# Optimization experiments

Hardware: AMD Instinct MI355X
Metric: run time of the kernel (lower is better)

## Reference

```python
import jax, jax.numpy as jnp
import numpy as np

N_EMB = 1024
N_HEADS = 16
HS = N_EMB // N_HEADS  # 64
BASE = 10000.0


def _rope_cache(T):
    # theta uses dim = n_emb (as in the source), sliced to hs//2 frequencies
    i = jnp.arange(HS // 2, dtype=jnp.float32)
    theta = BASE ** (-2.0 * i / N_EMB)            # [hs/2]
    pos = jnp.arange(T, dtype=jnp.float32)        # [T]
    ang = pos[:, None] * theta[None, :]           # [T, hs/2]
    return jnp.cos(ang), jnp.sin(ang)


def _apply_rope(x, cos, sin):
    # x: [B, T, nh, hs]; rotate consecutive pairs along hs
    b, t, nh, hs = x.shape
    xr = x.reshape(b, t, nh, hs // 2, 2)
    c = cos[None, :, None, :]
    s = sin[None, :, None, :]
    r0 = xr[..., 0] * c - xr[..., 1] * s
    r1 = xr[..., 1] * c + xr[..., 0] * s
    return jnp.stack([r0, r1], axis=-1).reshape(b, t, nh, hs)


def setup_inputs() -> dict:
    key = jax.random.key(0)
    k1, k2, k3, k4 = jax.random.split(key, 4)
    B, T = 2, 2048
    w_std = 0.02
    x = jax.random.normal(k1, (B, T, N_EMB), jnp.float32)
    Wq = jax.random.normal(k2, (N_EMB, N_EMB), jnp.float32) * w_std
    Wk = jax.random.normal(k3, (N_EMB, N_EMB), jnp.float32) * w_std
    Wv = jax.random.normal(k4, (N_EMB, N_EMB), jnp.float32) * w_std
    return {"x": x, "Wq": Wq, "Wk": Wk, "Wv": Wv}


def reference(x, Wq, Wk, Wv):
    B, T, C = x.shape
    # nn.Linear(bias=False): y = x @ W.T
    q = (x @ Wq.T).reshape(B, T, N_HEADS, HS)
    k = (x @ Wk.T).reshape(B, T, N_HEADS, HS)
    v = (x @ Wv.T).reshape(B, T, N_HEADS, HS)
    cos, sin = _rope_cache(T)
    q = _apply_rope(q, cos, sin)
    k = _apply_rope(k, cos, sin)
    # scale uses C (n_emb), as in the source (not head_size)
    wei = jnp.einsum('bqhd,bkhd->bhqk', q, k) * (C ** -0.5)  # [B, nh, T, T]
    mask = jnp.tril(jnp.ones((T, T), dtype=bool))
    wei = jnp.where(mask[None, None], wei, -jnp.inf)
    wei = jax.nn.softmax(wei, axis=-1)
    # dropout is identity in eval mode
    out = jnp.einsum('bhqk,bkhd->bqhd', wei, v).reshape(B, T, C)
    return out
```

## Files before the change

### kernel.cpp

```cpp
#include <hip/hip_runtime.h>
#include <stdint.h>

typedef unsigned short u16;
typedef __bf16 bf16x8 __attribute__((ext_vector_type(8)));
typedef unsigned short u16x8 __attribute__((ext_vector_type(8)));
typedef float f32x4 __attribute__((ext_vector_type(4)));
typedef uint32_t u32v4 __attribute__((ext_vector_type(4)));

#define LOG2E 1.4426950408889634f

typedef const __attribute__((address_space(1))) uint32_t as1_u32;
typedef __attribute__((address_space(3))) uint32_t as3_u32;

__device__ __forceinline__ u16 f2bf(float f) {
  union { float f; uint32_t i; } v; v.f = f;
  uint32_t r = (v.i + 0x7fffu + ((v.i >> 16) & 1u)) >> 16;
  return (u16)r;
}
__device__ __forceinline__ float bf2f(u16 u) {
  union { uint32_t i; float f; } v; v.i = ((uint32_t)u) << 16; return v.f;
}

__device__ __forceinline__ void gld_lds16(const void* g, void* l) {
  as1_u32* gp = (as1_u32*)((uintptr_t)g);
  as3_u32* lp = (as3_u32*)(uint32_t)(uintptr_t)(l);
  __builtin_amdgcn_global_load_lds(gp, lp, 16, 0, 0);
}

__device__ __forceinline__ float fast_exp2(float x) {
  float r;
  asm("v_exp_f32 %0, %1" : "=v"(r) : "v"(x));
  return r;
}

__global__ __launch_bounds__(256) void f32_to_bf16(
    const float* __restrict__ x, const float* __restrict__ wq,
    const float* __restrict__ wk, const float* __restrict__ wv,
    u16* __restrict__ xc, u16* __restrict__ wqc,
    u16* __restrict__ wkc, u16* __restrict__ wvc) {
  const int z = blockIdx.y;
  const float* src = z == 0 ? x : (z == 1 ? wq : (z == 2 ? wk : wv));
  u16* dst = z == 0 ? xc : (z == 1 ? wqc : (z == 2 ? wkc : wvc));
  const int n = z == 0 ? (1 << 22) : (1 << 20);

  const int idx = (blockIdx.x * 256 + (int)threadIdx.x) * 8;
  if (idx >= n) return;
  const f32x4 a = *(const f32x4*)&src[idx];
  const f32x4 b = *(const f32x4*)&src[idx + 4];
  u16x8 o;
#pragma unroll
  for (int j = 0; j < 4; j++) { o[j] = f2bf(a[j]); o[j + 4] = f2bf(b[j]); }
  *(u16x8*)&dst[idx] = o;
}

__global__ __launch_bounds__(256) void qkv_gemm(
    const u16* __restrict__ xc, const u16* __restrict__ wqc,
    const u16* __restrict__ wkc, const u16* __restrict__ wvc,
    u16* __restrict__ qo, u16* __restrict__ ko, u16* __restrict__ vt) {
  __shared__ __align__(16) u16 As[128 * 64];
  __shared__ __align__(16) u16 Bs[128 * 64];

  const int tid = threadIdx.x;
  const int lane = tid & 63;
  const int w = tid >> 6;
  const int wm = w >> 1, wn = w & 1;
  const int quad = lane >> 4, m16 = lane & 15;
  const int which = blockIdx.z;

  const u16* __restrict__ Ap;
  const u16* __restrict__ Bp;
  int m0, n0;
  if (which == 2) {
    Ap = wvc; Bp = xc;
    m0 = blockIdx.x * 128;
    n0 = blockIdx.y * 128;
  } else {
    Ap = xc; Bp = which == 0 ? wqc : wkc;
    m0 = blockIdx.y * 128;
    n0 = blockIdx.x * 128;
  }

  const f32x4 z4 = {0.f, 0.f, 0.f, 0.f};
  f32x4 acc[4][4];
#pragma unroll
  for (int i = 0; i < 4; i++)
#pragma unroll
    for (int j = 0; j < 4; j++) acc[i][j] = z4;

  const int lrow = lane >> 3;
  const int scol = ((lane & 7) ^ (lrow & 7)) * 8;
  const int srowA = m0 + w * 32 + lrow;
  const int srowB = n0 + w * 32 + lrow;
  const int rsw = m16 & 7;

  for (int k0 = 0; k0 < 1024; k0 += 64) {
    __syncthreads();
#pragma unroll
    for (int j = 0; j < 4; j++) {
      gld_lds16(&Ap[(size_t)(srowA + j * 8) * 1024 + k0 + scol],
                &As[(w * 32 + j * 8) * 64]);
      gld_lds16(&Bp[(size_t)(srowB + j * 8) * 1024 + k0 + scol],
                &Bs[(w * 32 + j * 8) * 64]);
    }
    __syncthreads();

#pragma unroll
    for (int kk = 0; kk < 2; kk++) {
      bf16x8 af[4], bfr[4];
#pragma unroll
      for (int t = 0; t < 4; t++) {
        af[t] = *(const bf16x8*)
            &As[(wm * 64 + t * 16 + m16) * 64 + (((kk * 4 + quad) ^ rsw) * 8)];
        bfr[t] = *(const bf16x8*)
            &Bs[(wn * 64 + t * 16 + m16) * 64 + (((kk * 4 + quad) ^ rsw) * 8)];
      }
#pragma unroll
      for (int mt = 0; mt < 4; mt++)
#pragma unroll
        for (int nt = 0; nt < 4; nt++)
          acc[mt][nt] = __builtin_amdgcn_mfma_f32_16x16x32_bf16(
              af[mt], bfr[nt], acc[mt][nt], 0, 0, 0);
    }
  }

  if (which < 2) {
    u16* __restrict__ out = which == 0 ? qo : ko;
    float th[4];
#pragma unroll
    for (int nt = 0; nt < 4; nt++) {
      const int i = ((nt * 16 + m16) & 63) >> 1;
      th[nt] = fast_exp2(-(float)i * 0.02595256324130752f)
               * 0.15915494309189535f;
    }
    const float sgn = (m16 & 1) ? 1.f : -1.f;
#pragma unroll
    for (int mt = 0; mt < 4; mt++) {
      const int row = m0 + wm * 64 + mt * 16 + quad * 4;
#pragma unroll
      for (int nt = 0; nt < 4; nt++) {
        const int n = n0 + wn * 64 + nt * 16 + m16;
        f32x4 a = acc[mt][nt];
#pragma unroll
        for (int r = 0; r < 4; r++) {
          const int t = (row + r) & 2047;
          const float rev = (float)t * th[nt];
          float fr, sv, cv;
          asm("v_fract_f32 %0, %1" : "=v"(fr) : "v"(rev));
          asm("v_sin_f32 %0, %1" : "=v"(sv) : "v"(fr));
          asm("v_cos_f32 %0, %1" : "=v"(cv) : "v"(fr));
          const float own = a[r];
          const float other = __shfl_xor(own, 1);
          out[(size_t)(row + r) * 1024 + n] = f2bf(own * cv + other * (sgn * sv));
        }
      }
    }
  } else {
    const int m16p = (m16 & 3) | ((m16 & 4) << 1) | ((m16 & 8) >> 1);
#pragma unroll
    for (int mt = 0; mt < 4; mt++) {
      const int row = m0 + wm * 64 + mt * 16 + quad * 4;
#pragma unroll
      for (int nt = 0; nt < 4; nt++) {
        const int n = n0 + wn * 64 + nt * 16 + m16p;
        f32x4 a = acc[mt][nt];
#pragma unroll
        for (int r = 0; r < 4; r++)
          vt[(size_t)(row + r) * 4096 + n] = f2bf(a[r]);
      }
    }
  }
}

__global__ __launch_bounds__(256, 2) void flash_attn(
    const u16* __restrict__ qg, const u16* __restrict__ kg,
    const u16* __restrict__ vt, float* __restrict__ out) {
  __shared__ __align__(16) u16 Ks[128 * 72];
  __shared__ __align__(16) u16 Vs[64 * 136];

  const int tid = threadIdx.x, lane = tid & 63, w = tid >> 6;
  const int quad = lane >> 4, m16 = lane & 15;

  const int id   = (int)blockIdx.x;
  const int X    = id & 7;
  const int rem  = id >> 3;
  const int s    = rem & 1;
  const int vloc = (rem >> 1) & 3;
  const int kk_  = rem >> 3;
  const int Q    = s ? 15 - kk_ : kk_;
  const int v    = X * 4 + vloc;
  const int h    = v & 15;
  const int b    = v >> 4;

  const size_t base  = (size_t)b * 2048 * 1024 + (size_t)h * 64;
  const size_t vbase = (size_t)(h * 64) * 4096 + (size_t)b * 2048;
  const float SC = 0.03125f * LOG2E;
  const f32x4 z4 = {0.f, 0.f, 0.f, 0.f};
  const int srow = tid >> 2, sc = (tid & 3) * 16;

  union { u16x8 u; bf16x8 f; } ones;
#pragma unroll
  for (int k = 0; k < 8; k++) ones.u[k] = 0x3F80;

  const int q0 = Q * 128;
  const int nr = Q + 1;

  const u16* qsA = &qg[base + (size_t)(q0 + w * 32 + m16) * 1024 + quad * 8];
  const bf16x8 qfA0 = *(const bf16x8*)qsA;
  const bf16x8 qfA1 = *(const bf16x8*)(qsA + 32);
  const u16* qsB = qsA + (size_t)16 * 1024;
  const bf16x8 qfB0 = *(const bf16x8*)qsB;
  const bf16x8 qfB1 = *(const bf16x8*)(qsB + 32);

  u16x8 kr0, kr1, kr2, kr3, vr0, vr1, vr2, vr3;
  {
    const u16* ks = &kg[base + (size_t)srow * 1024 + sc];
    kr0 = *(const u16x8*)ks; kr1 = *(const u16x8*)(ks + 8);
    const u16* ks2 = ks + (size_t)64 * 1024;
    kr2 = *(const u16x8*)ks2; kr3 = *(const u16x8*)(ks2 + 8);
    const u16* vs = &vt[vbase + (size_t)srow * 4096 + sc];
    vr0 = *(const u16x8*)vs; vr1 = *(const u16x8*)(vs + 8);
    vr2 = *(const u16x8*)(vs + 64); vr3 = *(const u16x8*)(vs + 72);
  }

  f32x4 lA = z4, lB = z4;
  f32x4 OA[4], OB[4];
#pragma unroll
  for (int d = 0; d < 4; d++) { OA[d] = z4; OB[d] = z4; }

  const int qrowA = q0 + w * 32 + quad * 4;
  const int qcolA = q0 + w * 32 + m16;

  for (int rr = 0; rr < nr; ++rr) {
    const int k0 = rr * 128;
    if (rr) __syncthreads();
    *(u16x8*)&Ks[srow * 72 + sc] = kr0;
    *(u16x8*)&Ks[srow * 72 + sc + 8] = kr1;
    *(u16x8*)&Ks[(64 + srow) * 72 + sc] = kr2;
    *(u16x8*)&Ks[(64 + srow) * 72 + sc + 8] = kr3;
    *(u16x8*)&Vs[srow * 136 + sc] = vr0;
    *(u16x8*)&Vs[srow * 136 + sc + 8] = vr1;
    *(u16x8*)&Vs[srow * 136 + 64 + sc] = vr2;
    *(u16x8*)&Vs[srow * 136 + 64 + sc + 8] = vr3;
    __syncthreads();
    if (rr + 1 < nr) {
      const u16* ks = &kg[base + (size_t)(k0 + 128 + srow) * 1024 + sc];
      kr0 = *(const u16x8*)ks; kr1 = *(const u16x8*)(ks + 8);
      const u16* ks2 = ks + (size_t)64 * 1024;
      kr2 = *(const u16x8*)ks2; kr3 = *(const u16x8*)(ks2 + 8);
      const u16* vs = &vt[vbase + (size_t)srow * 4096 + k0 + 128 + sc];
      vr0 = *(const u16x8*)vs; vr1 = *(const u16x8*)(vs + 8);
      vr2 = *(const u16x8*)(vs + 64); vr3 = *(const u16x8*)(vs + 72);
    }

    f32x4 SA[8], SB[8];
#pragma unroll
    for (int nt = 0; nt < 8; nt++) {
      const bf16x8 kf0 = *(const bf16x8*)&Ks[(nt * 16 + m16) * 72 + quad * 8];
      const bf16x8 kf1 =
          *(const bf16x8*)&Ks[(nt * 16 + m16) * 72 + 32 + quad * 8];
      SA[nt] = __builtin_amdgcn_mfma_f32_16x16x32_bf16(kf0, qfA0, z4, 0, 0, 0);
      SA[nt] = __builtin_amdgcn_mfma_f32_16x16x32_bf16(kf1, qfA1, SA[nt], 0, 0, 0);
      SB[nt] = __builtin_amdgcn_mfma_f32_16x16x32_bf16(kf0, qfB0, z4, 0, 0, 0);
      SB[nt] = __builtin_amdgcn_mfma_f32_16x16x32_bf16(kf1, qfB1, SB[nt], 0, 0, 0);
    }

    const bool lastr = (rr == nr - 1);

    union { u32v4 u; bf16x8 f; } PA[4], PB[4];
    {
      uint32_t W[16];
#pragma unroll
      for (int nt = 0; nt < 8; nt++) {
        float p[4];
#pragma unroll
        for (int r = 0; r < 4; r++) {
          float e = fast_exp2(SA[nt][r] * SC);
          const int key = k0 + nt * 16 + quad * 4 + r;
          if (lastr && key > qcolA) e = 0.f;
          p[r] = e;
        }
        uint32_t w0, w1;
        asm("v_cvt_pk_bf16_f32 %0, %1, %2" : "=v"(w0) : "v"(p[0]), "v"(p[1]));
        asm("v_cvt_pk_bf16_f32 %0, %1, %2" : "=v"(w1) : "v"(p[2]), "v"(p[3]));
        W[2 * nt] = w0; W[2 * nt + 1] = w1;
      }
#pragma unroll
      for (int ks = 0; ks < 4; ks++) {
        uint32_t a0 = W[4 * ks], b0 = W[4 * ks + 2];
        uint32_t a1 = W[4 * ks + 1], b1 = W[4 * ks + 3];
        asm("v_permlane32_swap_b32 %0, %1" : "+v"(a0), "+v"(b0));
        asm("v_permlane32_swap_b32 %0, %1" : "+v"(a1), "+v"(b1));
        PA[ks].u = (u32v4){a0, a1, b0, b1};
      }
    }
    {
      const int qcolB = qcolA + 16;
      uint32_t W[16];
#pragma unroll
      for (int nt = 0; nt < 8; nt++) {
        float p[4];
#pragma unroll
        for (int r = 0; r < 4; r++) {
          float e = fast_exp2(SB[nt][r] * SC);
          const int key = k0 + nt * 16 + quad * 4 + r;
          if (lastr && key > qcolB) e = 0.f;
          p[r] = e;
        }
        uint32_t w0, w1;
        asm("v_cvt_pk_bf16_f32 %0, %1, %2" : "=v"(w0) : "v"(p[0]), "v"(p[1]));
        asm("v_cvt_pk_bf16_f32 %0, %1, %2" : "=v"(w1) : "v"(p[2]), "v"(p[3]));
        W[2 * nt] = w0; W[2 * nt + 1] = w1;
      }
#pragma unroll
      for (int ks = 0; ks < 4; ks++) {
        uint32_t a0 = W[4 * ks], b0 = W[4 * ks + 2];
        uint32_t a1 = W[4 * ks + 1], b1 = W[4 * ks + 3];
        asm("v_permlane32_swap_b32 %0, %1" : "+v"(a0), "+v"(b0));
        asm("v_permlane32_swap_b32 %0, %1" : "+v"(a1), "+v"(b1));
        PB[ks].u = (u32v4){a0, a1, b0, b1};
      }
    }

#pragma unroll
    for (int ks = 0; ks < 4; ks++) {
      lA = __builtin_amdgcn_mfma_f32_16x16x32_bf16(PA[ks].f, ones.f, lA, 0, 0, 0);
      lB = __builtin_amdgcn_mfma_f32_16x16x32_bf16(PB[ks].f, ones.f, lB, 0, 0, 0);
    }

#pragma unroll
    for (int dt = 0; dt < 4; dt++) {
#pragma unroll
      for (int ks = 0; ks < 4; ks++) {
        const bf16x8 vf =
            *(const bf16x8*)&Vs[(dt * 16 + m16) * 136 + ks * 32 + quad * 8];
        OA[dt] = __builtin_amdgcn_mfma_f32_16x16x32_bf16(PA[ks].f, vf, OA[dt],
                                                         0, 0, 0);
        OB[dt] = __builtin_amdgcn_mfma_f32_16x16x32_bf16(PB[ks].f, vf, OB[dt],
                                                         0, 0, 0);
      }
    }
  }

  float invA[4], invB[4];
#pragma unroll
  for (int r = 0; r < 4; r++) { invA[r] = 1.0f / lA[r]; invB[r] = 1.0f / lB[r]; }

#pragma unroll
  for (int dt = 0; dt < 4; dt++)
#pragma unroll
    for (int r = 0; r < 4; r++) {
      out[base + (size_t)(qrowA + r) * 1024 + dt * 16 + m16] =
          OA[dt][r] * invA[r];
      out[base + (size_t)(qrowA + 16 + r) * 1024 + dt * 16 + m16] =
          OB[dt][r] * invB[r];
    }
}

extern "C" void kernel_launch(void* const* d_in, const int* in_sizes, int n_in,
                              void* d_out, int out_size, void* d_ws, size_t ws_size,
                              hipStream_t stream) {
  const float* x  = (const float*)d_in[0];
  const float* Wq = (const float*)d_in[1];
  const float* Wk = (const float*)d_in[2];
  const float* Wv = (const float*)d_in[3];
  u16* qb  = (u16*)d_ws;
  u16* kb  = qb  + (size_t)4096 * 1024;
  u16* vtw = kb  + (size_t)4096 * 1024;
  u16* xc  = vtw + (size_t)4096 * 1024;
  u16* wqc = xc  + (size_t)4096 * 1024;
  u16* wkc = wqc + (size_t)1024 * 1024;
  u16* wvc = wkc + (size_t)1024 * 1024;

  f32_to_bf16<<<dim3(2048, 4), 256, 0, stream>>>(x, Wq, Wk, Wv,
                                                 xc, wqc, wkc, wvc);
  qkv_gemm<<<dim3(8, 32, 3), 256, 0, stream>>>(xc, wqc, wkc, wvc,
                                               qb, kb, vtw);
  flash_attn<<<dim3(512, 1, 1), 256, 0, stream>>>(qb, kb, vtw, (float*)d_out);
}
```

Baseline: 162.0 us.

## Split RoPE into separate kernel, remap GEMM grid per XCD, double-buffer attention LDS

Three changes. The QKV GEMM now uses a flat 1D grid whose block index is remapped so that consecutive blocks on the same XCD share row panels, aiming at better L2 reuse. RoPE moves out of the GEMM epilogue into a separate in-place elementwise kernel, which drops the per-element sin/cos and shuffle from the GEMM but costs an extra launch and an extra read/write pass over Q and K. Flash attention double-buffers its K/V shared-memory tiles so each iteration needs one barrier instead of two, at the cost of twice the LDS per block, which may affect occupancy.

```diff
diff --git a/kernel.cpp b/kernel.cpp
--- a/kernel.cpp
+++ b/kernel.cpp
@@ -65,19 +65,26 @@
   const int w = tid >> 6;
   const int wm = w >> 1, wn = w & 1;
   const int quad = lane >> 4, m16 = lane & 15;
-  const int which = blockIdx.z;
+
+  const int id    = (int)blockIdx.x;
+  const int xcd   = id & 7;
+  const int local = id >> 3;
+  const int by    = xcd * 4 + (local & 3);
+  const int rest  = local >> 2;
+  const int which = rest % 3;
+  const int bx    = rest / 3;
 
   const u16* __restrict__ Ap;
   const u16* __restrict__ Bp;
   int m0, n0;
   if (which == 2) {
     Ap = wvc; Bp = xc;
-    m0 = blockIdx.x * 128;
-    n0 = blockIdx.y * 128;
+    m0 = bx * 128;
+    n0 = by * 128;
   } else {
     Ap = xc; Bp = which == 0 ? wqc : wkc;
-    m0 = blockIdx.y * 128;
-    n0 = blockIdx.x * 128;
+    m0 = by * 128;
+    n0 = bx * 128;
   }
 
   const f32x4 z4 = {0.f, 0.f, 0.f, 0.f};
@@ -125,14 +132,6 @@
 
   if (which < 2) {
     u16* __restrict__ out = which == 0 ? qo : ko;
-    float th[4];
-#pragma unroll
-    for (int nt = 0; nt < 4; nt++) {
-      const int i = ((nt * 16 + m16) & 63) >> 1;
-      th[nt] = fast_exp2(-(float)i * 0.02595256324130752f)
-               * 0.15915494309189535f;
-    }
-    const float sgn = (m16 & 1) ? 1.f : -1.f;
 #pragma unroll
     for (int mt = 0; mt < 4; mt++) {
       const int row = m0 + wm * 64 + mt * 16 + quad * 4;
@@ -141,17 +140,8 @@
         const int n = n0 + wn * 64 + nt * 16 + m16;
         f32x4 a = acc[mt][nt];
 #pragma unroll
-        for (int r = 0; r < 4; r++) {
-          const int t = (row + r) & 2047;
-          const float rev = (float)t * th[nt];
-          float fr, sv, cv;
-          asm("v_fract_f32 %0, %1" : "=v"(fr) : "v"(rev));
-          asm("v_sin_f32 %0, %1" : "=v"(sv) : "v"(fr));
-          asm("v_cos_f32 %0, %1" : "=v"(cv) : "v"(fr));
-          const float own = a[r];
-          const float other = __shfl_xor(own, 1);
-          out[(size_t)(row + r) * 1024 + n] = f2bf(own * cv + other * (sgn * sv));
-        }
+        for (int r = 0; r < 4; r++)
+          out[(size_t)(row + r) * 1024 + n] = f2bf(a[r]);
       }
     }
   } else {
@@ -171,11 +161,39 @@
   }
 }
 
+__global__ __launch_bounds__(256) void rope_inplace(u16* __restrict__ qb,
+                                                    u16* __restrict__ kb) {
+  u16* buf = blockIdx.y == 0 ? qb : kb;
+  const int p = blockIdx.x * 256 + (int)threadIdx.x;
+  const int e0 = p * 8;
+  const int row = e0 >> 10;
+  const int col0 = e0 & 1023;
+  const int t = row & 2047;
+  const float tf = (float)t;
+
+  u16x8 d = *(const u16x8*)&buf[(size_t)row * 1024 + col0];
+  u16x8 o;
+#pragma unroll
+  for (int j = 0; j < 4; j++) {
+    const int i = ((col0 & 63) >> 1) + j;
+    const float th = fast_exp2(-(float)i * 0.02595256324130752f);
+    const float rev = tf * th * 0.15915494309189535f;
+    float fr, s, c;
+    asm("v_fract_f32 %0, %1" : "=v"(fr) : "v"(rev));
+    asm("v_sin_f32 %0, %1" : "=v"(s) : "v"(fr));
+    asm("v_cos_f32 %0, %1" : "=v"(c) : "v"(fr));
+    const float a0 = bf2f(d[2 * j]), a1 = bf2f(d[2 * j + 1]);
+    o[2 * j]     = f2bf(a0 * c - a1 * s);
+    o[2 * j + 1] = f2bf(a1 * c + a0 * s);
+  }
+  *(u16x8*)&buf[(size_t)row * 1024 + col0] = o;
+}
+
 __global__ __launch_bounds__(256, 2) void flash_attn(
     const u16* __restrict__ qg, const u16* __restrict__ kg,
     const u16* __restrict__ vt, float* __restrict__ out) {
-  __shared__ __align__(16) u16 Ks[128 * 72];
-  __shared__ __align__(16) u16 Vs[64 * 136];
+  __shared__ __align__(16) u16 Ks[2][128 * 72];
+  __shared__ __align__(16) u16 Vs[2][64 * 136];
 
   const int tid = threadIdx.x, lane = tid & 63, w = tid >> 6;
   const int quad = lane >> 4, m16 = lane & 15;
@@ -230,18 +248,19 @@
   const int qrowA = q0 + w * 32 + quad * 4;
   const int qcolA = q0 + w * 32 + m16;
 
+  int p = 0;
   for (int rr = 0; rr < nr; ++rr) {
     const int k0 = rr * 128;
-    if (rr) __syncthreads();
-    *(u16x8*)&Ks[srow * 72 + sc] = kr0;
-    *(u16x8*)&Ks[srow * 72 + sc + 8] = kr1;
-    *(u16x8*)&Ks[(64 + srow) * 72 + sc] = kr2;
-    *(u16x8*)&Ks[(64 + srow) * 72 + sc + 8] = kr3;
-    *(u16x8*)&Vs[srow * 136 + sc] = vr0;
-    *(u16x8*)&Vs[srow * 136 + sc + 8] = vr1;
-    *(u16x8*)&Vs[srow * 136 + 64 + sc] = vr2;
-    *(u16x8*)&Vs[srow * 136 + 64 + sc + 8] = vr3;
-    __syncthreads();
+    u16* ksp = &Ks[p][0];
+    u16* vsp = &Vs[p][0];
+    *(u16x8*)&ksp[srow * 72 + sc] = kr0;
+    *(u16x8*)&ksp[srow * 72 + sc + 8] = kr1;
+    *(u16x8*)&ksp[(64 + srow) * 72 + sc] = kr2;
+    *(u16x8*)&ksp[(64 + srow) * 72 + sc + 8] = kr3;
+    *(u16x8*)&vsp[srow * 136 + sc] = vr0;
+    *(u16x8*)&vsp[srow * 136 + sc + 8] = vr1;
+    *(u16x8*)&vsp[srow * 136 + 64 + sc] = vr2;
+    *(u16x8*)&vsp[srow * 136 + 64 + sc + 8] = vr3;
     if (rr + 1 < nr) {
       const u16* ks = &kg[base + (size_t)(k0 + 128 + srow) * 1024 + sc];
       kr0 = *(const u16x8*)ks; kr1 = *(const u16x8*)(ks + 8);
@@ -251,13 +270,14 @@
       vr0 = *(const u16x8*)vs; vr1 = *(const u16x8*)(vs + 8);
       vr2 = *(const u16x8*)(vs + 64); vr3 = *(const u16x8*)(vs + 72);
     }
+    __syncthreads();
 
     f32x4 SA[8], SB[8];
 #pragma unroll
     for (int nt = 0; nt < 8; nt++) {
-      const bf16x8 kf0 = *(const bf16x8*)&Ks[(nt * 16 + m16) * 72 + quad * 8];
+      const bf16x8 kf0 = *(const bf16x8*)&ksp[(nt * 16 + m16) * 72 + quad * 8];
       const bf16x8 kf1 =
-          *(const bf16x8*)&Ks[(nt * 16 + m16) * 72 + 32 + quad * 8];
+          *(const bf16x8*)&ksp[(nt * 16 + m16) * 72 + 32 + quad * 8];
       SA[nt] = __builtin_amdgcn_mfma_f32_16x16x32_bf16(kf0, qfA0, z4, 0, 0, 0);
       SA[nt] = __builtin_amdgcn_mfma_f32_16x16x32_bf16(kf1, qfA1, SA[nt], 0, 0, 0);
       SB[nt] = __builtin_amdgcn_mfma_f32_16x16x32_bf16(kf0, qfB0, z4, 0, 0, 0);
@@ -271,17 +291,17 @@
       uint32_t W[16];
 #pragma unroll
       for (int nt = 0; nt < 8; nt++) {
-        float p[4];
+        float pe[4];
 #pragma unroll
         for (int r = 0; r < 4; r++) {
           float e = fast_exp2(SA[nt][r] * SC);
           const int key = k0 + nt * 16 + quad * 4 + r;
           if (lastr && key > qcolA) e = 0.f;
-          p[r] = e;
+          pe[r] = e;
         }
         uint32_t w0, w1;
-        asm("v_cvt_pk_bf16_f32 %0, %1, %2" : "=v"(w0) : "v"(p[0]), "v"(p[1]));
-        asm("v_cvt_pk_bf16_f32 %0, %1, %2" : "=v"(w1) : "v"(p[2]), "v"(p[3]));
+        asm("v_cvt_pk_bf16_f32 %0, %1, %2" : "=v"(w0) : "v"(pe[0]), "v"(pe[1]));
+        asm("v_cvt_pk_bf16_f32 %0, %1, %2" : "=v"(w1) : "v"(pe[2]), "v"(pe[3]));
         W[2 * nt] = w0; W[2 * nt + 1] = w1;
       }
 #pragma unroll
@@ -298,17 +318,17 @@
       uint32_t W[16];
 #pragma unroll
       for (int nt = 0; nt < 8; nt++) {
-        float p[4];
+        float pe[4];
 #pragma unroll
         for (int r = 0; r < 4; r++) {
           float e = fast_exp2(SB[nt][r] * SC);
           const int key = k0 + nt * 16 + quad * 4 + r;
           if (lastr && key > qcolB) e = 0.f;
-          p[r] = e;
+          pe[r] = e;
         }
         uint32_t w0, w1;
-        asm("v_cvt_pk_bf16_f32 %0, %1, %2" : "=v"(w0) : "v"(p[0]), "v"(p[1]));
-        asm("v_cvt_pk_bf16_f32 %0, %1, %2" : "=v"(w1) : "v"(p[2]), "v"(p[3]));
+        asm("v_cvt_pk_bf16_f32 %0, %1, %2" : "=v"(w0) : "v"(pe[0]), "v"(pe[1]));
+        asm("v_cvt_pk_bf16_f32 %0, %1, %2" : "=v"(w1) : "v"(pe[2]), "v"(pe[3]));
         W[2 * nt] = w0; W[2 * nt + 1] = w1;
       }
 #pragma unroll
@@ -332,13 +352,14 @@
 #pragma unroll
       for (int ks = 0; ks < 4; ks++) {
         const bf16x8 vf =
-            *(const bf16x8*)&Vs[(dt * 16 + m16) * 136 + ks * 32 + quad * 8];
+            *(const bf16x8*)&vsp[(dt * 16 + m16) * 136 + ks * 32 + quad * 8];
         OA[dt] = __builtin_amdgcn_mfma_f32_16x16x32_bf16(PA[ks].f, vf, OA[dt],
                                                          0, 0, 0);
         OB[dt] = __builtin_amdgcn_mfma_f32_16x16x32_bf16(PB[ks].f, vf, OB[dt],
                                                          0, 0, 0);
       }
     }
+    p ^= 1;
   }
 
   float invA[4], invB[4];
@@ -373,7 +394,8 @@
 
   f32_to_bf16<<<dim3(2048, 4), 256, 0, stream>>>(x, Wq, Wk, Wv,
                                                  xc, wqc, wkc, wvc);
-  qkv_gemm<<<dim3(8, 32, 3), 256, 0, stream>>>(xc, wqc, wkc, wvc,
-                                               qb, kb, vtw);
+  qkv_gemm<<<dim3(768, 1, 1), 256, 0, stream>>>(xc, wqc, wkc, wvc,
+                                                qb, kb, vtw);
+  rope_inplace<<<dim3(2048, 2), 256, 0, stream>>>(qb, kb);
   flash_attn<<<dim3(512, 1, 1), 256, 0, stream>>>(qb, kb, vtw, (float*)d_out);
 }
```

After: 152.7 us. 1.06x faster.
